# Optimization experiments

Measured on AMD Instinct MI355X. Metric: run time of the kernel, lower is better.

The kernel has to match this reference:

```python
import jax, jax.numpy as jnp
import numpy as np

B, T, P, H, D = 8, 16, 14, 16, 64
L = P * P            # 196 patches (CLS excluded)
DM = H * D           # 1024 = d_model
NS = 16              # n_synos
T2 = T * T           # 256 = n_frames**2


def _conv2d(x, w, b):
    # x: [N,C,H,W], w: [O,I,kh,kw], stride 1, SAME padding (ksize//2 for odd k)
    y = jax.lax.conv_general_dilated(x, w, (1, 1), 'SAME',
                                     dimension_numbers=('NCHW', 'OIHW', 'NCHW'))
    return y + b[None, :, None, None]


def _layernorm(x, g, b):
    m = x.mean(-1, keepdims=True)
    v = x.var(-1, keepdims=True)
    return (x - m) / jnp.sqrt(v + 1e-5) * g + b


def setup_inputs() -> dict:
    key = jax.random.key(0)
    ks = jax.random.split(key, 12)
    q = jax.random.normal(ks[0], (B, T, L + 1, H, D), jnp.float32)
    k = jax.random.normal(ks[1], (B, T, L + 1, H, D), jnp.float32)
    v = jax.random.normal(ks[2], (B, T, L + 1, H, D), jnp.float32)
    syno_emb = jax.random.normal(ks[3], (NS, DM), jnp.float32) * 0.02
    t_conv_w = jax.random.normal(ks[4], (1, 2 * H, 3, 3), jnp.float32) * 0.001
    t_conv_b = jnp.zeros((1,), jnp.float32)
    ln_g = jnp.ones((T2,), jnp.float32)
    ln_b = jnp.zeros((T2,), jnp.float32)
    w1 = jax.random.normal(ks[5], (T2, T2), jnp.float32) * 0.02
    b1 = jnp.zeros((T2,), jnp.float32)
    w2 = jax.random.normal(ks[6], (T2, T2), jnp.float32) * 0.02
    b2 = jnp.zeros((T2,), jnp.float32)
    p_conv_w = jax.random.normal(ks[7], (1, T2, 3, 3), jnp.float32) * 0.001
    p_conv_b = jnp.zeros((1,), jnp.float32)
    return dict(q=q, k=k, v=v, syno_emb=syno_emb,
                t_conv_w=t_conv_w, t_conv_b=t_conv_b,
                ln_g=ln_g, ln_b=ln_b, w1=w1, b1=b1, w2=w2, b2=b2,
                p_conv_w=p_conv_w, p_conv_b=p_conv_b)


def reference(q, k, v, syno_emb, t_conv_w, t_conv_b, ln_g, ln_b,
              w1, b1, w2, b2, p_conv_w, p_conv_b):
    # ---------------- temporal detection ----------------
    def head_aff(a):  # a: [B,T,L,H,D] -> [B*L, H, T, T]
        a = a.transpose(0, 2, 1, 3, 4)  # [B,L,T,H,D]
        scale = 1.0 / (a.shape[-1] ** 0.5)
        aff = jnp.einsum('nlqhc,nlkhc->nlqkh', a * scale, a)  # [B,L,T,T,H]
        aff = jax.nn.softmax(aff, axis=-2)  # softmax over key frames
        return aff.reshape(B * L, T, T, H).transpose(0, 3, 1, 2)

    affs = jnp.concatenate([head_aff(q[:, :, 1:]), head_aff(k[:, :, 1:])],
                           axis=1)                      # [B*L, 2H, T, T]
    aff = _conv2d(affs, t_conv_w, t_conv_b)             # [B*L, 1, T, T]
    aff = aff.reshape(B, P, P, T2)                      # [B, P, P, T^2]
    h = _layernorm(aff, ln_g, ln_b)
    h = h @ w1.T + b1
    h = jax.nn.gelu(h, approximate=False)               # torch nn.GELU default
    h = h @ w2.T + b2
    aff = aff + h
    aff = aff.transpose(0, 3, 1, 2)                     # [B, T^2, P, P]
    aff = _conv2d(aff, p_conv_w, p_conv_b)              # [B, 1, P, P]
    y_t = aff.reshape(B, -1)                            # [B, P*P]

    # ---------------- spatial detection ----------------
    kf = k[:, :, 1:].reshape(B, T, L, DM)
    vf = v[:, :, 1:].reshape(B, T, L, DM)
    s_scale = 1.0 / (DM ** 0.5)
    s_aff = jnp.einsum('qw,ntkw->ntqk', syno_emb * s_scale, kf)  # [B,T,NS,L]
    s_aff = jax.nn.softmax(s_aff, axis=-1)
    s_mix = jnp.einsum('ntql,ntlw->ntqw', s_aff, vf)    # [B,T,NS,DM]
    y_s = s_mix.reshape(B, T * NS, DM).mean(axis=1)     # [B, DM]

    return (y_t, y_s)
```

## Files before the change

kernel.cpp:

```cpp
#include <hip/hip_runtime.h>
#include <hip/hip_bf16.h>
#include <math.h>

#define BB 8
#define TT 16
#define PP 14
#define LL 196
#define HH 16
#define DD 64
#define DM 1024
#define NS 16
#define T2 256
#define LP1 197

using bf16x8 = __attribute__((ext_vector_type(8))) short;
using f32x4  = __attribute__((ext_vector_type(4))) float;

__device__ __forceinline__ float dot4(float4 a, float4 b) {
    return a.x*b.x + a.y*b.y + a.z*b.z + a.w*b.w;
}

__device__ __forceinline__ uint32_t pkbf(float lo, float hi) {
    uint32_t a = __builtin_bit_cast(uint32_t, lo);
    uint32_t b = __builtin_bit_cast(uint32_t, hi);
    a += 0x7FFFu + ((a >> 16) & 1u);
    b += 0x7FFFu + ((b >> 16) & 1u);
    return (a >> 16) | (b & 0xFFFF0000u);
}

__device__ __forceinline__ void split2(float x, float y, uint32_t* h, uint32_t* lo) {
    const uint32_t hh = pkbf(x, y);
    const float hx = __builtin_bit_cast(float, hh << 16);
    const float hy = __builtin_bit_cast(float, hh & 0xFFFF0000u);
    *h = hh;
    *lo = pkbf(x - hx, y - hy);
}

__device__ __forceinline__ void pksplit(float4 p, float4 q, bf16x8& hi, bf16x8& lo) {
    uint32_t uh[4], ul[4];
    split2(p.x, p.y, &uh[0], &ul[0]);
    split2(p.z, p.w, &uh[1], &ul[1]);
    split2(q.x, q.y, &uh[2], &ul[2]);
    split2(q.z, q.w, &uh[3], &ul[3]);
    struct U4 { uint32_t v[4]; } th, tl;
    th.v[0] = uh[0]; th.v[1] = uh[1]; th.v[2] = uh[2]; th.v[3] = uh[3];
    tl.v[0] = ul[0]; tl.v[1] = ul[1]; tl.v[2] = ul[2]; tl.v[3] = ul[3];
    hi = __builtin_bit_cast(bf16x8, th);
    lo = __builtin_bit_cast(bf16x8, tl);
}

__global__ __launch_bounds__(256) void kprep(
        const float* __restrict__ syno,
        uint32_t* __restrict__ synoHi, uint32_t* __restrict__ synoLo) {
    const int i = blockIdx.x * 256 + threadIdx.x;
    const float x = syno[2 * i], y = syno[2 * i + 1];
    uint32_t h, lo;
    split2(x, y, &h, &lo);
    synoHi[i] = h;
    synoLo[i] = lo;
}

__global__ __launch_bounds__(256) void k1_temporal(
        const float* __restrict__ qin, const float* __restrict__ kin,
        const float* __restrict__ tw,  const float* __restrict__ tbv,
        const uint32_t* __restrict__ synoHi, const uint32_t* __restrict__ synoLo,
        float* __restrict__ affRaw, float* __restrict__ SLout) {
    __shared__ __align__(16) float lds_c[16 * 260];
    __shared__ __align__(16) float sl_part[4][16][16];

    const int bid = blockIdx.x, b = bid / LL, l = bid % LL;
    const int tid = threadIdx.x, wid = tid >> 6, lane = tid & 63;
    const int mrow = lane & 15;
    const int g = lane >> 4;
    const int colb = lane & 15;
    const int oq = tid >> 4, ok = tid & 15;

    const size_t rowbase = ((size_t)(b*TT + mrow)*LP1 + 1 + l)*DM + g*8;
    f32x4 acc_sl = {0.f, 0.f, 0.f, 0.f};
    float accv = tbv[0];

    #pragma unroll
    for (int pass = 0; pass < 2; ++pass) {
        #pragma unroll
        for (int jj = 0; jj < 2; ++jj) {
            const int j = pass * 2 + jj;
            #pragma unroll
            for (int hf = 0; hf < 2; ++hf) {
                const int ch = 2*wid + 8*j + hf;
                const float* sp2 = (pass == 0) ? qin : kin;
                const float* base = sp2 + rowbase + (size_t)(ch & 15)*DD;
                const float4 a0 = *reinterpret_cast<const float4*>(base);
                const float4 a1 = *reinterpret_cast<const float4*>(base + 4);
                const float4 a2 = *reinterpret_cast<const float4*>(base + 32);
                const float4 a3 = *reinterpret_cast<const float4*>(base + 36);
                bf16x8 h1, l1, h2, l2;
                pksplit(a0, a1, h1, l1);
                pksplit(a2, a3, h2, l2);
                f32x4 acc = {0.f, 0.f, 0.f, 0.f};
                acc = __builtin_amdgcn_mfma_f32_16x16x32_bf16(h1, h1, acc, 0, 0, 0);
                acc = __builtin_amdgcn_mfma_f32_16x16x32_bf16(h1, l1, acc, 0, 0, 0);
                acc = __builtin_amdgcn_mfma_f32_16x16x32_bf16(l1, h1, acc, 0, 0, 0);
                acc = __builtin_amdgcn_mfma_f32_16x16x32_bf16(h2, h2, acc, 0, 0, 0);
                acc = __builtin_amdgcn_mfma_f32_16x16x32_bf16(h2, l2, acc, 0, 0, 0);
                acc = __builtin_amdgcn_mfma_f32_16x16x32_bf16(l2, h2, acc, 0, 0, 0);
                if (pass == 1) {
                    const int off = colb * 512 + (ch - 16) * 32 + g * 4;
                    const bf16x8 sh1 = *reinterpret_cast<const bf16x8*>(synoHi + off);
                    const bf16x8 sl1 = *reinterpret_cast<const bf16x8*>(synoLo + off);
                    const bf16x8 sh2 = *reinterpret_cast<const bf16x8*>(synoHi + off + 16);
                    const bf16x8 sl2 = *reinterpret_cast<const bf16x8*>(synoLo + off + 16);
                    acc_sl = __builtin_amdgcn_mfma_f32_16x16x32_bf16(h1, sh1, acc_sl, 0, 0, 0);
                    acc_sl = __builtin_amdgcn_mfma_f32_16x16x32_bf16(h1, sl1, acc_sl, 0, 0, 0);
                    acc_sl = __builtin_amdgcn_mfma_f32_16x16x32_bf16(l1, sh1, acc_sl, 0, 0, 0);
                    acc_sl = __builtin_amdgcn_mfma_f32_16x16x32_bf16(h2, sh2, acc_sl, 0, 0, 0);
                    acc_sl = __builtin_amdgcn_mfma_f32_16x16x32_bf16(h2, sl2, acc_sl, 0, 0, 0);
                    acc_sl = __builtin_amdgcn_mfma_f32_16x16x32_bf16(l2, sh2, acc_sl, 0, 0, 0);
                }
                const float x0 = acc[0]*0.125f, x1 = acc[1]*0.125f;
                const float x2 = acc[2]*0.125f, x3 = acc[3]*0.125f;
                float m0 = x0, m1 = x1, m2 = x2, m3 = x3;
                #pragma unroll
                for (int msk = 1; msk < 16; msk <<= 1) {
                    m0 = fmaxf(m0, __shfl_xor(m0, msk, 64));
                    m1 = fmaxf(m1, __shfl_xor(m1, msk, 64));
                    m2 = fmaxf(m2, __shfl_xor(m2, msk, 64));
                    m3 = fmaxf(m3, __shfl_xor(m3, msk, 64));
                }
                const float e0 = __expf(x0 - m0), e1 = __expf(x1 - m1);
                const float e2 = __expf(x2 - m2), e3 = __expf(x3 - m3);
                float s0 = e0, s1 = e1, s2 = e2, s3 = e3;
                #pragma unroll
                for (int msk = 1; msk < 16; msk <<= 1) {
                    s0 += __shfl_xor(s0, msk, 64);
                    s1 += __shfl_xor(s1, msk, 64);
                    s2 += __shfl_xor(s2, msk, 64);
                    s3 += __shfl_xor(s3, msk, 64);
                }
                const int slot = 2*wid + 8*jj + hf;
                float* cp = lds_c + slot * 260;
                cp[(g*4 + 0)*16 + colb] = e0 / s0;
                cp[(g*4 + 1)*16 + colb] = e1 / s1;
                cp[(g*4 + 2)*16 + colb] = e2 / s2;
                cp[(g*4 + 3)*16 + colb] = e3 / s3;
            }
        }
        if (pass == 1) {
            #pragma unroll
            for (int r = 0; r < 4; ++r)
                sl_part[wid][g * 4 + r][colb] = acc_sl[r];
        }
        __syncthreads();
        #pragma unroll
        for (int ky = 0; ky < 3; ++ky) {
            const int iq = oq + ky - 1;
            if (iq < 0 || iq > 15) continue;
            #pragma unroll
            for (int kx = 0; kx < 3; ++kx) {
                const int ik = ok + kx - 1;
                if (ik < 0 || ik > 15) continue;
                const int pix = iq * 16 + ik;
                #pragma unroll
                for (int s = 0; s < 16; ++s)
                    accv += lds_c[s * 260 + pix] * tw[(pass*16 + s)*9 + ky*3 + kx];
            }
        }
        if (pass == 0) __syncthreads();
    }
    affRaw[(size_t)bid * T2 + tid] = accv;

    {
        const int t = tid >> 4, qq = tid & 15;
        const float s = sl_part[0][t][qq] + sl_part[1][t][qq] +
                        sl_part[2][t][qq] + sl_part[3][t][qq];
        SLout[((size_t)(b * TT + t) * NS + qq) * LL + l] = s * 0.03125f;
    }
}

__global__ __launch_bounds__(256) void k2_mlp(
        const float* __restrict__ affRaw,
        const float* __restrict__ lng, const float* __restrict__ lnb,
        const float* __restrict__ w1, const float* __restrict__ b1,
        const float* __restrict__ w2, const float* __restrict__ b2,
        float* __restrict__ affRes) {
    __shared__ __align__(16) float lx[4 * 256];
    __shared__ __align__(16) float lln[4 * 256];
    __shared__ __align__(16) float lg[4 * 256];
    const int tid = threadIdx.x;
    const int wave = tid >> 6, lane = tid & 63;
    const int i0 = blockIdx.x * 4;
    {
        const float* xr = affRaw + (size_t)(i0 + wave) * 256;
        float4 x = reinterpret_cast<const float4*>(xr)[lane];
        float sm = x.x + x.y + x.z + x.w;
        float ss = x.x * x.x + x.y * x.y + x.z * x.z + x.w * x.w;
        #pragma unroll
        for (int m = 1; m < 64; m <<= 1) {
            sm += __shfl_xor(sm, m, 64);
            ss += __shfl_xor(ss, m, 64);
        }
        const float mean = sm * (1.f / 256.f);
        const float var = ss * (1.f / 256.f) - mean * mean;
        const float inv = rsqrtf(var + 1e-5f);
        const float4 g4 = reinterpret_cast<const float4*>(lng)[lane];
        const float4 bb = reinterpret_cast<const float4*>(lnb)[lane];
        float4 ln;
        ln.x = (x.x - mean) * inv * g4.x + bb.x;
        ln.y = (x.y - mean) * inv * g4.y + bb.y;
        ln.z = (x.z - mean) * inv * g4.z + bb.z;
        ln.w = (x.w - mean) * inv * g4.w + bb.w;
        reinterpret_cast<float4*>(lx + wave * 256)[lane] = x;
        reinterpret_cast<float4*>(lln + wave * 256)[lane] = ln;
    }
    __syncthreads();
    const int j = tid;
    float a0 = 0.f, a1 = 0.f, a2 = 0.f, a3 = 0.f;
    {
        const float4* wr = reinterpret_cast<const float4*>(w1 + (size_t)j * 256);
        const float4* l0 = reinterpret_cast<const float4*>(lln);
        const float4* l1 = reinterpret_cast<const float4*>(lln + 256);
        const float4* l2 = reinterpret_cast<const float4*>(lln + 512);
        const float4* l3 = reinterpret_cast<const float4*>(lln + 768);
        #pragma unroll 8
        for (int m4 = 0; m4 < 64; ++m4) {
            const float4 w = wr[m4];
            a0 += dot4(w, l0[m4]); a1 += dot4(w, l1[m4]);
            a2 += dot4(w, l2[m4]); a3 += dot4(w, l3[m4]);
        }
    }
    const float bj = b1[j];
    const float kInvSqrt2 = 0.70710678118654752f;
    float h0 = a0 + bj, h1 = a1 + bj, h2 = a2 + bj, h3 = a3 + bj;
    lg[0 * 256 + j] = 0.5f * h0 * (1.f + erff(h0 * kInvSqrt2));
    lg[1 * 256 + j] = 0.5f * h1 * (1.f + erff(h1 * kInvSqrt2));
    lg[2 * 256 + j] = 0.5f * h2 * (1.f + erff(h2 * kInvSqrt2));
    lg[3 * 256 + j] = 0.5f * h3 * (1.f + erff(h3 * kInvSqrt2));
    __syncthreads();
    a0 = a1 = a2 = a3 = 0.f;
    {
        const float4* wr = reinterpret_cast<const float4*>(w2 + (size_t)j * 256);
        const float4* l0 = reinterpret_cast<const float4*>(lg);
        const float4* l1 = reinterpret_cast<const float4*>(lg + 256);
        const float4* l2 = reinterpret_cast<const float4*>(lg + 512);
        const float4* l3 = reinterpret_cast<const float4*>(lg + 768);
        #pragma unroll 8
        for (int m4 = 0; m4 < 64; ++m4) {
            const float4 w = wr[m4];
            a0 += dot4(w, l0[m4]); a1 += dot4(w, l1[m4]);
            a2 += dot4(w, l2[m4]); a3 += dot4(w, l3[m4]);
        }
    }
    const float b2j = b2[j];
    affRes[(size_t)(i0 + 0) * 256 + j] = lx[0 * 256 + j] + a0 + b2j;
    affRes[(size_t)(i0 + 1) * 256 + j] = lx[1 * 256 + j] + a1 + b2j;
    affRes[(size_t)(i0 + 2) * 256 + j] = lx[2 * 256 + j] + a2 + b2j;
    affRes[(size_t)(i0 + 3) * 256 + j] = lx[3 * 256 + j] + a3 + b2j;
}

__global__ __launch_bounds__(256) void k3a_pconv(
        const float* __restrict__ affRes, const float* __restrict__ pw,
        float* __restrict__ part) {
    __shared__ __align__(16) float lpw[576];
    const int b = blockIdx.x >> 2, cc = blockIdx.x & 3;
    const int tid = threadIdx.x;
    for (int idx = tid; idx < 576; idx += 256) {
        const int kk = idx / 64, c = idx & 63;
        lpw[kk * 64 + c] = pw[(size_t)(cc * 64 + c) * 9 + kk];
    }
    __syncthreads();
    if (tid < 196) {
        const int p1 = tid / 14, p2 = tid % 14;
        float s = 0.f;
        #pragma unroll
        for (int ky = 0; ky < 3; ++ky) {
            const int ip1 = p1 + ky - 1;
            if (ip1 < 0 || ip1 > 13) continue;
            #pragma unroll
            for (int kx = 0; kx < 3; ++kx) {
                const int ip2 = p2 + kx - 1;
                if (ip2 < 0 || ip2 > 13) continue;
                const float4* ar = reinterpret_cast<const float4*>(
                    affRes + (size_t)(b * LL + ip1 * 14 + ip2) * 256 + cc * 64);
                const float4* wr = reinterpret_cast<const float4*>(lpw + (ky * 3 + kx) * 64);
                #pragma unroll
                for (int c4 = 0; c4 < 16; ++c4) s += dot4(ar[c4], wr[c4]);
            }
        }
        part[(cc * 8 + b) * 196 + tid] = s;
    }
}

__global__ void k3b_yt(const float* __restrict__ part,
                       const float* __restrict__ pcb, float* __restrict__ out) {
    const int b = blockIdx.x, tid = threadIdx.x;
    if (tid < 196) {
        float s = pcb[0];
        #pragma unroll
        for (int cc = 0; cc < 4; ++cc) s += part[(cc * 8 + b) * 196 + tid];
        out[b * 196 + tid] = s;
    }
}

__global__ __launch_bounds__(256) void k4b_softmax(
        const float* __restrict__ SL, float* __restrict__ WSUM) {
    __shared__ float lp[16 * 200];
    const int t = blockIdx.x, b = blockIdx.y;
    const int tid = threadIdx.x;
    const int qq = tid >> 4, j = tid & 15;
    const float* row = SL + (size_t)((b * TT + t) * NS + qq) * LL;
    float v[13];
    float m = -1e30f;
    #pragma unroll
    for (int i = 0; i < 13; ++i) {
        const int l = j + i * 16;
        v[i] = (l < LL) ? row[l] : -1e30f;
        m = fmaxf(m, v[i]);
    }
    #pragma unroll
    for (int msk = 1; msk < 16; msk <<= 1) m = fmaxf(m, __shfl_xor(m, msk, 64));
    float s = 0.f;
    #pragma unroll
    for (int i = 0; i < 13; ++i) {
        const int l = j + i * 16;
        v[i] = (l < LL) ? __expf(v[i] - m) : 0.f;
        s += v[i];
    }
    #pragma unroll
    for (int msk = 1; msk < 16; msk <<= 1) s += __shfl_xor(s, msk, 64);
    const float inv = 1.f / s;
    #pragma unroll
    for (int i = 0; i < 13; ++i) {
        const int l = j + i * 16;
        if (l < LL) lp[qq * 200 + l] = v[i] * inv;
    }
    __syncthreads();
    if (tid < LL) {
        float w = 0.f;
        #pragma unroll
        for (int qi = 0; qi < 16; ++qi) w += lp[qi * 200 + tid];
        WSUM[(size_t)(b * TT + t) * LL + tid] = w;
    }
}

__global__ __launch_bounds__(256) void k4c_vsum(
        const float* __restrict__ vin, const float* __restrict__ WSUM,
        float* __restrict__ PS) {
    __shared__ float lw[98];
    const int t = blockIdx.x, b = blockIdx.y, z = blockIdx.z;
    const int tid = threadIdx.x;
    const int bt = b * TT + t;
    if (tid < 98) lw[tid] = WSUM[(size_t)bt * LL + z * 98 + tid];
    __syncthreads();
    float4 acc = make_float4(0.f, 0.f, 0.f, 0.f);
    const float* vb = vin + ((size_t)bt * LP1 + 1 + z * 98) * DM + tid * 4;
    #pragma unroll 4
    for (int l = 0; l < 98; ++l) {
        const float4 v = *reinterpret_cast<const float4*>(vb + (size_t)l * DM);
        const float w = lw[l];
        acc.x += w * v.x; acc.y += w * v.y; acc.z += w * v.z; acc.w += w * v.w;
    }
    *reinterpret_cast<float4*>(PS + ((size_t)bt * 2 + z) * DM + tid * 4) = acc;
}

__global__ void k4d_ys(const float* __restrict__ PS, float* __restrict__ out) {
    const int i = blockIdx.x * 256 + threadIdx.x;
    const int b = i >> 10, w = i & 1023;
    float s = 0.f;
    #pragma unroll
    for (int tz = 0; tz < 32; ++tz) s += PS[((size_t)b * 32 + tz) * DM + w];
    out[1568 + i] = s * (1.f / 256.f);
}

extern "C" void kernel_launch(void* const* d_in, const int* in_sizes, int n_in,
                              void* d_out, int out_size, void* d_ws, size_t ws_size,
                              hipStream_t stream) {
    const float* q    = (const float*)d_in[0];
    const float* k    = (const float*)d_in[1];
    const float* v    = (const float*)d_in[2];
    const float* syno = (const float*)d_in[3];
    const float* tw   = (const float*)d_in[4];
    const float* tbv  = (const float*)d_in[5];
    const float* lng  = (const float*)d_in[6];
    const float* lnb  = (const float*)d_in[7];
    const float* w1   = (const float*)d_in[8];
    const float* b1   = (const float*)d_in[9];
    const float* w2   = (const float*)d_in[10];
    const float* b2   = (const float*)d_in[11];
    const float* pw   = (const float*)d_in[12];
    const float* pcb  = (const float*)d_in[13];
    float* out = (float*)d_out;

    float* ws = (float*)d_ws;
    float* affRaw = ws;
    float* affRes = ws + 401408;
    float* SL     = ws + 802816;
    float* WSUM   = ws + 1204224;
    float* part   = ws + 1229312;
    uint32_t* synoHi = (uint32_t*)(ws + 1235584);
    uint32_t* synoLo = (uint32_t*)(ws + 1243776);
    float* PS     = ws;

    hipLaunchKernelGGL(kprep, dim3(32), dim3(256), 0, stream, syno, synoHi, synoLo);
    hipLaunchKernelGGL(k1_temporal, dim3(BB * LL), dim3(256), 0, stream,
                       q, k, tw, tbv, synoHi, synoLo, affRaw, SL);
    hipLaunchKernelGGL(k2_mlp, dim3(392), dim3(256), 0, stream,
                       affRaw, lng, lnb, w1, b1, w2, b2, affRes);
    hipLaunchKernelGGL(k3a_pconv, dim3(32), dim3(256), 0, stream,
                       affRes, pw, part);
    hipLaunchKernelGGL(k3b_yt, dim3(8), dim3(256), 0, stream, part, pcb, out);
    hipLaunchKernelGGL(k4b_softmax, dim3(16, 8), dim3(256), 0, stream, SL, WSUM);
    hipLaunchKernelGGL(k4c_vsum, dim3(16, 8, 2), dim3(256), 0, stream, v, WSUM, PS);
    hipLaunchKernelGGL(k4d_ys, dim3(32), dim3(256), 0, stream, PS, out);
}
```

Measured before the change: 149.3 us.

## Widen temporal kernel to 1024 threads, one wave per head pair

Block size for the temporal-affinity kernel goes from 256 to 1024 threads. Sixteen waves now each handle two heads of q or k at once, replacing the two sequential passes. The 3x3 conv over 32 channels is split across four thread groups of 8 channels, with partial sums reduced through shared memory. This raises memory-level parallelism and drops one barrier phase, at the cost of more LDS per block, an extra reduction step and possibly lower block residency.

```diff
diff --git a/kernel.cpp b/kernel.cpp
--- a/kernel.cpp
+++ b/kernel.cpp
@@ -60,119 +60,122 @@
     synoLo[i] = lo;
 }
 
-__global__ __launch_bounds__(256) void k1_temporal(
+__global__ __launch_bounds__(1024, 8) void k1_temporal(
         const float* __restrict__ qin, const float* __restrict__ kin,
         const float* __restrict__ tw,  const float* __restrict__ tbv,
         const uint32_t* __restrict__ synoHi, const uint32_t* __restrict__ synoLo,
         float* __restrict__ affRaw, float* __restrict__ SLout) {
-    __shared__ __align__(16) float lds_c[16 * 260];
-    __shared__ __align__(16) float sl_part[4][16][16];
+    __shared__ __align__(16) float lds_c[32 * 260];
+    __shared__ __align__(16) float sl_part[8][16][16];
+    __shared__ __align__(16) float cpart[4][256];
 
     const int bid = blockIdx.x, b = bid / LL, l = bid % LL;
     const int tid = threadIdx.x, wid = tid >> 6, lane = tid & 63;
     const int mrow = lane & 15;
     const int g = lane >> 4;
     const int colb = lane & 15;
-    const int oq = tid >> 4, ok = tid & 15;
-
+    const bool kside = (wid >= 8);
+    const float* sp2 = kside ? kin : qin;
     const size_t rowbase = ((size_t)(b*TT + mrow)*LP1 + 1 + l)*DM + g*8;
+
     f32x4 acc_sl = {0.f, 0.f, 0.f, 0.f};
-    float accv = tbv[0];
-
-    #pragma unroll
-    for (int pass = 0; pass < 2; ++pass) {
-        #pragma unroll
-        for (int jj = 0; jj < 2; ++jj) {
-            const int j = pass * 2 + jj;
+
+    #pragma unroll
+    for (int it = 0; it < 2; ++it) {
+        const int hd = ((wid & 7) << 1) + it;
+        const float* base = sp2 + rowbase + (size_t)hd * DD;
+        const float4 a0 = *reinterpret_cast<const float4*>(base);
+        const float4 a1 = *reinterpret_cast<const float4*>(base + 4);
+        const float4 a2 = *reinterpret_cast<const float4*>(base + 32);
+        const float4 a3 = *reinterpret_cast<const float4*>(base + 36);
+        bf16x8 h1, l1, h2, l2;
+        pksplit(a0, a1, h1, l1);
+        pksplit(a2, a3, h2, l2);
+        f32x4 acc = {0.f, 0.f, 0.f, 0.f};
+        acc = __builtin_amdgcn_mfma_f32_16x16x32_bf16(h1, h1, acc, 0, 0, 0);
+        acc = __builtin_amdgcn_mfma_f32_16x16x32_bf16(h1, l1, acc, 0, 0, 0);
+        acc = __builtin_amdgcn_mfma_f32_16x16x32_bf16(l1, h1, acc, 0, 0, 0);
+        acc = __builtin_amdgcn_mfma_f32_16x16x32_bf16(h2, h2, acc, 0, 0, 0);
+        acc = __builtin_amdgcn_mfma_f32_16x16x32_bf16(h2, l2, acc, 0, 0, 0);
+        acc = __builtin_amdgcn_mfma_f32_16x16x32_bf16(l2, h2, acc, 0, 0, 0);
+        if (kside) {
+            const int off = colb * 512 + hd * 32 + g * 4;
+            const bf16x8 sh1 = *reinterpret_cast<const bf16x8*>(synoHi + off);
+            const bf16x8 sv1 = *reinterpret_cast<const bf16x8*>(synoLo + off);
+            const bf16x8 sh2 = *reinterpret_cast<const bf16x8*>(synoHi + off + 16);
+            const bf16x8 sv2 = *reinterpret_cast<const bf16x8*>(synoLo + off + 16);
+            acc_sl = __builtin_amdgcn_mfma_f32_16x16x32_bf16(h1, sh1, acc_sl, 0, 0, 0);
+            acc_sl = __builtin_amdgcn_mfma_f32_16x16x32_bf16(h1, sv1, acc_sl, 0, 0, 0);
+            acc_sl = __builtin_amdgcn_mfma_f32_16x16x32_bf16(l1, sh1, acc_sl, 0, 0, 0);
+            acc_sl = __builtin_amdgcn_mfma_f32_16x16x32_bf16(h2, sh2, acc_sl, 0, 0, 0);
+            acc_sl = __builtin_amdgcn_mfma_f32_16x16x32_bf16(h2, sv2, acc_sl, 0, 0, 0);
+            acc_sl = __builtin_amdgcn_mfma_f32_16x16x32_bf16(l2, sh2, acc_sl, 0, 0, 0);
+        }
+        const float x0 = acc[0]*0.125f, x1 = acc[1]*0.125f;
+        const float x2 = acc[2]*0.125f, x3 = acc[3]*0.125f;
+        float m0 = x0, m1 = x1, m2 = x2, m3 = x3;
+        #pragma unroll
+        for (int msk = 1; msk < 16; msk <<= 1) {
+            m0 = fmaxf(m0, __shfl_xor(m0, msk, 64));
+            m1 = fmaxf(m1, __shfl_xor(m1, msk, 64));
+            m2 = fmaxf(m2, __shfl_xor(m2, msk, 64));
+            m3 = fmaxf(m3, __shfl_xor(m3, msk, 64));
+        }
+        const float e0 = __expf(x0 - m0), e1 = __expf(x1 - m1);
+        const float e2 = __expf(x2 - m2), e3 = __expf(x3 - m3);
+        float s0 = e0, s1 = e1, s2 = e2, s3 = e3;
+        #pragma unroll
+        for (int msk = 1; msk < 16; msk <<= 1) {
+            s0 += __shfl_xor(s0, msk, 64);
+            s1 += __shfl_xor(s1, msk, 64);
+            s2 += __shfl_xor(s2, msk, 64);
+            s3 += __shfl_xor(s3, msk, 64);
+        }
+        const int ch = (kside ? 16 : 0) + hd;
+        float* cp = lds_c + ch * 260;
+        cp[(g*4 + 0)*16 + colb] = e0 / s0;
+        cp[(g*4 + 1)*16 + colb] = e1 / s1;
+        cp[(g*4 + 2)*16 + colb] = e2 / s2;
+        cp[(g*4 + 3)*16 + colb] = e3 / s3;
+    }
+    if (kside) {
+        #pragma unroll
+        for (int r = 0; r < 4; ++r)
+            sl_part[wid - 8][g * 4 + r][colb] = acc_sl[r];
+    }
+    __syncthreads();
+
+    const int pix = tid & 255, grp = tid >> 8;
+    const int oq = pix >> 4, ok = pix & 15;
+    float accv = 0.f;
+    #pragma unroll
+    for (int ky = 0; ky < 3; ++ky) {
+        const int iq = oq + ky - 1;
+        if (iq < 0 || iq > 15) continue;
+        #pragma unroll
+        for (int kx = 0; kx < 3; ++kx) {
+            const int ik = ok + kx - 1;
+            if (ik < 0 || ik > 15) continue;
+            const int p2 = iq * 16 + ik;
             #pragma unroll
-            for (int hf = 0; hf < 2; ++hf) {
-                const int ch = 2*wid + 8*j + hf;
-                const float* sp2 = (pass == 0) ? qin : kin;
-                const float* base = sp2 + rowbase + (size_t)(ch & 15)*DD;
-                const float4 a0 = *reinterpret_cast<const float4*>(base);
-                const float4 a1 = *reinterpret_cast<const float4*>(base + 4);
-                const float4 a2 = *reinterpret_cast<const float4*>(base + 32);
-                const float4 a3 = *reinterpret_cast<const float4*>(base + 36);
-                bf16x8 h1, l1, h2, l2;
-                pksplit(a0, a1, h1, l1);
-                pksplit(a2, a3, h2, l2);
-                f32x4 acc = {0.f, 0.f, 0.f, 0.f};
-                acc = __builtin_amdgcn_mfma_f32_16x16x32_bf16(h1, h1, acc, 0, 0, 0);
-                acc = __builtin_amdgcn_mfma_f32_16x16x32_bf16(h1, l1, acc, 0, 0, 0);
-                acc = __builtin_amdgcn_mfma_f32_16x16x32_bf16(l1, h1, acc, 0, 0, 0);
-                acc = __builtin_amdgcn_mfma_f32_16x16x32_bf16(h2, h2, acc, 0, 0, 0);
-                acc = __builtin_amdgcn_mfma_f32_16x16x32_bf16(h2, l2, acc, 0, 0, 0);
-                acc = __builtin_amdgcn_mfma_f32_16x16x32_bf16(l2, h2, acc, 0, 0, 0);
-                if (pass == 1) {
-                    const int off = colb * 512 + (ch - 16) * 32 + g * 4;
-                    const bf16x8 sh1 = *reinterpret_cast<const bf16x8*>(synoHi + off);
-                    const bf16x8 sl1 = *reinterpret_cast<const bf16x8*>(synoLo + off);
-                    const bf16x8 sh2 = *reinterpret_cast<const bf16x8*>(synoHi + off + 16);
-                    const bf16x8 sl2 = *reinterpret_cast<const bf16x8*>(synoLo + off + 16);
-                    acc_sl = __builtin_amdgcn_mfma_f32_16x16x32_bf16(h1, sh1, acc_sl, 0, 0, 0);
-                    acc_sl = __builtin_amdgcn_mfma_f32_16x16x32_bf16(h1, sl1, acc_sl, 0, 0, 0);
-                    acc_sl = __builtin_amdgcn_mfma_f32_16x16x32_bf16(l1, sh1, acc_sl, 0, 0, 0);
-                    acc_sl = __builtin_amdgcn_mfma_f32_16x16x32_bf16(h2, sh2, acc_sl, 0, 0, 0);
-                    acc_sl = __builtin_amdgcn_mfma_f32_16x16x32_bf16(h2, sl2, acc_sl, 0, 0, 0);
-                    acc_sl = __builtin_amdgcn_mfma_f32_16x16x32_bf16(l2, sh2, acc_sl, 0, 0, 0);
-                }
-                const float x0 = acc[0]*0.125f, x1 = acc[1]*0.125f;
-                const float x2 = acc[2]*0.125f, x3 = acc[3]*0.125f;
-                float m0 = x0, m1 = x1, m2 = x2, m3 = x3;
-                #pragma unroll
-                for (int msk = 1; msk < 16; msk <<= 1) {
-                    m0 = fmaxf(m0, __shfl_xor(m0, msk, 64));
-                    m1 = fmaxf(m1, __shfl_xor(m1, msk, 64));
-                    m2 = fmaxf(m2, __shfl_xor(m2, msk, 64));
-                    m3 = fmaxf(m3, __shfl_xor(m3, msk, 64));
-                }
-                const float e0 = __expf(x0 - m0), e1 = __expf(x1 - m1);
-                const float e2 = __expf(x2 - m2), e3 = __expf(x3 - m3);
-                float s0 = e0, s1 = e1, s2 = e2, s3 = e3;
-                #pragma unroll
-                for (int msk = 1; msk < 16; msk <<= 1) {
-                    s0 += __shfl_xor(s0, msk, 64);
-                    s1 += __shfl_xor(s1, msk, 64);
-                    s2 += __shfl_xor(s2, msk, 64);
-                    s3 += __shfl_xor(s3, msk, 64);
-                }
-                const int slot = 2*wid + 8*jj + hf;
-                float* cp = lds_c + slot * 260;
-                cp[(g*4 + 0)*16 + colb] = e0 / s0;
-                cp[(g*4 + 1)*16 + colb] = e1 / s1;
-                cp[(g*4 + 2)*16 + colb] = e2 / s2;
-                cp[(g*4 + 3)*16 + colb] = e3 / s3;
+            for (int c = 0; c < 8; ++c) {
+                const int ch = grp * 8 + c;
+                accv += lds_c[ch * 260 + p2] * tw[ch * 9 + ky * 3 + kx];
             }
         }
-        if (pass == 1) {
-            #pragma unroll
-            for (int r = 0; r < 4; ++r)
-                sl_part[wid][g * 4 + r][colb] = acc_sl[r];
-        }
-        __syncthreads();
-        #pragma unroll
-        for (int ky = 0; ky < 3; ++ky) {
-            const int iq = oq + ky - 1;
-            if (iq < 0 || iq > 15) continue;
-            #pragma unroll
-            for (int kx = 0; kx < 3; ++kx) {
-                const int ik = ok + kx - 1;
-                if (ik < 0 || ik > 15) continue;
-                const int pix = iq * 16 + ik;
-                #pragma unroll
-                for (int s = 0; s < 16; ++s)
-                    accv += lds_c[s * 260 + pix] * tw[(pass*16 + s)*9 + ky*3 + kx];
-            }
-        }
-        if (pass == 0) __syncthreads();
-    }
-    affRaw[(size_t)bid * T2 + tid] = accv;
-
-    {
+    }
+    cpart[grp][pix] = accv;
+    if (tid < 256) {
         const int t = tid >> 4, qq = tid & 15;
-        const float s = sl_part[0][t][qq] + sl_part[1][t][qq] +
-                        sl_part[2][t][qq] + sl_part[3][t][qq];
+        float s = 0.f;
+        #pragma unroll
+        for (int w8 = 0; w8 < 8; ++w8) s += sl_part[w8][t][qq];
         SLout[((size_t)(b * TT + t) * NS + qq) * LL + l] = s * 0.03125f;
+    }
+    __syncthreads();
+    if (tid < 256) {
+        affRaw[(size_t)bid * T2 + tid] = tbv[0] + cpart[0][tid] + cpart[1][tid]
+                                       + cpart[2][tid] + cpart[3][tid];
     }
 }
 
@@ -400,7 +403,7 @@
     float* PS     = ws;
 
     hipLaunchKernelGGL(kprep, dim3(32), dim3(256), 0, stream, syno, synoHi, synoLo);
-    hipLaunchKernelGGL(k1_temporal, dim3(BB * LL), dim3(256), 0, stream,
+    hipLaunchKernelGGL(k1_temporal, dim3(BB * LL), dim3(1024), 0, stream,
                        q, k, tw, tbv, synoHi, synoLo, affRaw, SL);
     hipLaunchKernelGGL(k2_mlp, dim3(392), dim3(256), 0, stream,
                        affRaw, lng, lnb, w1, b1, w2, b2, affRes);
```

Measured after the change: 161.9 us. 1.08x slower.
